# Kernel optimization log

Measured on AMD Instinct MI355X. Metric: run time of the kernel, lower is better.

The kernel has to match this reference:

```python
import jax, jax.numpy as jnp
import numpy as np

N_POINTS = 2_000_000
OUTPUT_DIM = 8
L_RES = 128
H_RES = 1024


def _to_idx(c, size):
    # c in [-1, 1], align_corners=True mapping to pixel coords
    p = (c + 1.0) * 0.5 * (size - 1)
    i0 = jnp.floor(p)
    w = p - i0  # interpolation weight toward i1
    i0 = jnp.clip(i0.astype(jnp.int32), 0, size - 1)
    i1 = jnp.clip(i0 + 1, 0, size - 1)
    return i0, i1, w


def trilinear_sample(grid, coords):
    # grid: [C, D, H, W]; coords: [N, 3] with (x->W, y->H, z->D); returns [C, N]
    C, D, H, W = grid.shape
    x0, x1, wx = _to_idx(coords[:, 0], W)
    y0, y1, wy = _to_idx(coords[:, 1], H)
    z0, z1, wz = _to_idx(coords[:, 2], D)
    g = lambda zi, yi, xi: grid[:, zi, yi, xi]  # gather -> [C, N]
    out = (g(z0, y0, x0) * ((1 - wz) * (1 - wy) * (1 - wx))
           + g(z0, y0, x1) * ((1 - wz) * (1 - wy) * wx)
           + g(z0, y1, x0) * ((1 - wz) * wy * (1 - wx))
           + g(z0, y1, x1) * ((1 - wz) * wy * wx)
           + g(z1, y0, x0) * (wz * (1 - wy) * (1 - wx))
           + g(z1, y0, x1) * (wz * (1 - wy) * wx)
           + g(z1, y1, x0) * (wz * wy * (1 - wx))
           + g(z1, y1, x1) * (wz * wy * wx))
    return out


def bilinear_sample(plane, coords):
    # plane: [C, H, W]; coords: [N, 2] with (x->W, y->H); returns [C, N]
    C, H, W = plane.shape
    x0, x1, wx = _to_idx(coords[:, 0], W)
    y0, y1, wy = _to_idx(coords[:, 1], H)
    g = lambda yi, xi: plane[:, yi, xi]  # [C, N]
    out = (g(y0, x0) * ((1 - wy) * (1 - wx))
           + g(y0, x1) * ((1 - wy) * wx)
           + g(y1, x0) * (wy * (1 - wx))
           + g(y1, x1) * (wy * wx))
    return out


def setup_inputs() -> dict:
    key = jax.random.key(0)
    k1, k2, k3 = jax.random.split(key, 3)
    xyz = jax.random.uniform(k1, (N_POINTS, 3), dtype=jnp.float32)  # in [0,1) subset of [-1,1]
    L_grid = jax.random.normal(k2, (1, OUTPUT_DIM, L_RES, L_RES, L_RES), dtype=jnp.float32) * 0.1
    H_planes = jax.random.normal(k3, (3, OUTPUT_DIM, H_RES, H_RES), dtype=jnp.float32) * 0.1
    return {"xyz": xyz, "bound": 1, "L_grid": L_grid, "H_planes": H_planes}


def reference(xyz, bound, L_grid, H_planes):
    xyz_norm = xyz / bound  # [N, 3]
    L_out = trilinear_sample(L_grid[0], xyz_norm)  # [C, N]
    H_out = (bilinear_sample(H_planes[0], xyz_norm[:, jnp.array([0, 1])])
             + bilinear_sample(H_planes[1], xyz_norm[:, jnp.array([1, 2])])
             + bilinear_sample(H_planes[2], xyz_norm[:, jnp.array([2, 0])]))
    return (L_out + H_out).T  # [N, C]
```

## Files before the change

### kernel.cpp

```cpp
#include <hip/hip_runtime.h>

#define LRES 128
#define HRES 1024
#define NB 256
#define BTS 1024
#define NBUCK 512
#define RCAP 8192
#define TELEM 2048

static const int LVOX = LRES * LRES * LRES;
static const int PPIX = HRES * HRES;
static const int TV = LVOX + 3 * PPIX;

typedef float f32x4 __attribute__((ext_vector_type(4)));
typedef unsigned u32x4 __attribute__((ext_vector_type(4)));


__device__ __forceinline__ void to_idx(float c, int size, int& i0, int& i1, float& w) {
    float p = (c + 1.0f) * 0.5f * (float)(size - 1);
    float f = floorf(p);
    w = p - f;
    int i = (int)f;
    i0 = min(max(i, 0), size - 1);
    i1 = min(i0 + 1, size - 1);
}

__device__ __forceinline__ unsigned f2bf(float f) {
    unsigned u = __float_as_uint(f);
    return (u + 0x7FFFu + ((u >> 16) & 1u)) >> 16;
}
__device__ __forceinline__ float bflo(unsigned u) { return __uint_as_float(u << 16); }
__device__ __forceinline__ float bfhi(unsigned u) { return __uint_as_float(u & 0xFFFF0000u); }

__device__ __forceinline__ void fma8u(f32x4& a0, f32x4& a1, uint4 q, float w) {
    a0.x = fmaf(bflo(q.x), w, a0.x);
    a0.y = fmaf(bfhi(q.x), w, a0.y);
    a0.z = fmaf(bflo(q.y), w, a0.z);
    a0.w = fmaf(bfhi(q.y), w, a0.w);
    a1.x = fmaf(bflo(q.z), w, a1.x);
    a1.y = fmaf(bfhi(q.z), w, a1.y);
    a1.z = fmaf(bflo(q.w), w, a1.z);
    a1.w = fmaf(bfhi(q.w), w, a1.w);
}

__device__ __forceinline__ unsigned spread3(unsigned x) {
    x &= 0x3FFu;
    x = (x | (x << 16)) & 0x030000FFu;
    x = (x | (x << 8)) & 0x0300F00Fu;
    x = (x | (x << 4)) & 0x030C30C3u;
    x = (x | (x << 2)) & 0x09249249u;
    return x;
}
__device__ __forceinline__ unsigned morton21(float x, float y, float z) {
    int px = min(max((int)(x * 128.f), 0), 127);
    int py = min(max((int)(y * 128.f), 0), 127);
    int pz = min(max((int)(z * 128.f), 0), 127);
    return spread3(px) | (spread3(py) << 1) | (spread3(pz) << 2);
}

__device__ __forceinline__ void gl_lds16(const float* src, float* lds_dst) {
    __builtin_amdgcn_global_load_lds(
        (const __attribute__((address_space(1))) void*)src,
        (__attribute__((address_space(3))) void*)lds_dst, 16, 0, 0);
}

__global__ __launch_bounds__(BTS) void hist_k(const float* __restrict__ xyz,
                                              const int* __restrict__ boundp,
                                              unsigned* __restrict__ hmat, int N) {
    __shared__ unsigned h[NBUCK];
    int b = blockIdx.x;
    for (int i = threadIdx.x; i < NBUCK; i += BTS) h[i] = 0u;
    __syncthreads();
    float invb = 1.0f / (float)boundp[0];
    int NG = (N + 3) >> 2;
    for (int g = b * BTS + threadIdx.x; g < NG; g += NB * BTS) {
        int n0 = g << 2;
        if (n0 + 4 <= N) {
            f32x4 qa = *(const f32x4*)(xyz + (size_t)n0 * 3);
            f32x4 qb = *(const f32x4*)(xyz + (size_t)n0 * 3 + 4);
            f32x4 qc = *(const f32x4*)(xyz + (size_t)n0 * 3 + 8);
            atomicAdd(&h[morton21(qa.x * invb, qa.y * invb, qa.z * invb) >> 12], 1u);
            atomicAdd(&h[morton21(qa.w * invb, qb.x * invb, qb.y * invb) >> 12], 1u);
            atomicAdd(&h[morton21(qb.z * invb, qb.w * invb, qc.x * invb) >> 12], 1u);
            atomicAdd(&h[morton21(qc.y * invb, qc.z * invb, qc.w * invb) >> 12], 1u);
        } else {
            for (int n = n0; n < N; ++n) {
                float x = xyz[(size_t)3 * n + 0] * invb;
                float y = xyz[(size_t)3 * n + 1] * invb;
                float z = xyz[(size_t)3 * n + 2] * invb;
                atomicAdd(&h[morton21(x, y, z) >> 12], 1u);
            }
        }
    }
    __syncthreads();
    for (int i = threadIdx.x; i < NBUCK; i += BTS)
        hmat[(size_t)i * NB + b] = h[i];
}

__global__ __launch_bounds__(1024) void offsets_k(unsigned* __restrict__ hmat,
                                                  unsigned* __restrict__ bb) {
    __shared__ unsigned tot[NBUCK];
    __shared__ unsigned cbase[NBUCK];
    int t = threadIdx.x;
    unsigned run = 0;
    if (t < NBUCK) {
        u32x4* row = (u32x4*)(hmat + (size_t)t * NB);
        for (int ch = 0; ch < NB / 32; ++ch) {
            u32x4 q[8];
#pragma unroll
            for (int k = 0; k < 8; ++k) q[k] = row[ch * 8 + k];
#pragma unroll
            for (int k = 0; k < 8; ++k) {
                unsigned v0 = q[k].x, v1 = q[k].y, v2 = q[k].z, v3 = q[k].w;
                q[k].x = run; run += v0;
                q[k].y = run; run += v1;
                q[k].z = run; run += v2;
                q[k].w = run; run += v3;
                row[ch * 8 + k] = q[k];
            }
        }
        tot[t] = run;
    }
    __syncthreads();
    for (int o = 1; o < NBUCK; o <<= 1) {
        unsigned v = 0;
        if (t < NBUCK && t >= o) v = tot[t - o];
        __syncthreads();
        if (t < NBUCK) tot[t] += v;
        __syncthreads();
    }
    if (t < NBUCK) {
        unsigned excl = tot[t] - run;
        cbase[t] = excl;
        bb[t] = excl;
        if (t == NBUCK - 1) bb[NBUCK] = tot[t];
    }
    __syncthreads();
    u32x4* hm4 = (u32x4*)hmat;
    for (int idx = t; idx < NB * NBUCK / 4; idx += 1024) {
        u32x4 q = hm4[idx];
        unsigned cb = cbase[idx >> 6];
        q.x += cb; q.y += cb; q.z += cb; q.w += cb;
        hm4[idx] = q;
    }
}

__global__ __launch_bounds__(BTS) void scat_tr_k(const float* __restrict__ xyz,
                                                 const int* __restrict__ boundp,
                                                 const float* __restrict__ Lg,
                                                 const float* __restrict__ Hp,
                                                 const unsigned* __restrict__ hmat,
                                                 float4* __restrict__ s1,
                                                 u32x4* __restrict__ gclb,
                                                 u32x4* __restrict__ pclb, int N) {
    __shared__ float stage[8 * TELEM];
    int b = blockIdx.x;
    if (b < NB) {
        unsigned* cnt = (unsigned*)stage;
        for (int i = threadIdx.x; i < NBUCK; i += BTS)
            cnt[i] = hmat[(size_t)i * NB + b];
        __syncthreads();
        float invb = 1.0f / (float)boundp[0];
        int NG = (N + 3) >> 2;
        for (int g = b * BTS + threadIdx.x; g < NG; g += NB * BTS) {
            int n0 = g << 2;
            if (n0 + 4 <= N) {
                f32x4 qa = *(const f32x4*)(xyz + (size_t)n0 * 3);
                f32x4 qb = *(const f32x4*)(xyz + (size_t)n0 * 3 + 4);
                f32x4 qc = *(const f32x4*)(xyz + (size_t)n0 * 3 + 8);
                {
                    float x = qa.x * invb, y = qa.y * invb, z = qa.z * invb;
                    unsigned d = atomicAdd(&cnt[morton21(x, y, z) >> 12], 1u);
                    s1[d] = make_float4(x, y, z, __int_as_float(n0 + 0));
                }
                {
                    float x = qa.w * invb, y = qb.x * invb, z = qb.y * invb;
                    unsigned d = atomicAdd(&cnt[morton21(x, y, z) >> 12], 1u);
                    s1[d] = make_float4(x, y, z, __int_as_float(n0 + 1));
                }
                {
                    float x = qb.z * invb, y = qb.w * invb, z = qc.x * invb;
                    unsigned d = atomicAdd(&cnt[morton21(x, y, z) >> 12], 1u);
                    s1[d] = make_float4(x, y, z, __int_as_float(n0 + 2));
                }
                {
                    float x = qc.y * invb, y = qc.z * invb, z = qc.w * invb;
                    unsigned d = atomicAdd(&cnt[morton21(x, y, z) >> 12], 1u);
                    s1[d] = make_float4(x, y, z, __int_as_float(n0 + 3));
                }
            } else {
                for (int n = n0; n < N; ++n) {
                    float x = xyz[(size_t)3 * n + 0] * invb;
                    float y = xyz[(size_t)3 * n + 1] * invb;
                    float z = xyz[(size_t)3 * n + 2] * invb;
                    unsigned d = atomicAdd(&cnt[morton21(x, y, z) >> 12], 1u);
                    s1[d] = make_float4(x, y, z, __int_as_float(n));
                }
            }
        }
    } else {
        int tb = b - NB;
        size_t vbase = (size_t)tb * TELEM;
        const float* srcbase;
        size_t cstride;
        u32x4* dst;
        if (vbase < (size_t)LVOX) {
            srcbase = Lg + vbase;
            cstride = LVOX;
            dst = gclb + vbase;
        } else {
            size_t u = vbase - LVOX;
            int p = (int)(u >> 20);
            size_t r = u & (size_t)(PPIX - 1);
            srcbase = Hp + (size_t)p * 8 * PPIX + r;
            cstride = PPIX;
            dst = pclb + (size_t)p * PPIX + r;
        }
        int wave = threadIdx.x >> 6;
        int lane = threadIdx.x & 63;
        for (int k = wave; k < 64; k += BTS / 64) {
            int c = k >> 3, s = k & 7;
            gl_lds16(srcbase + (size_t)c * cstride + s * 256 + lane * 4,
                     &stage[k * 256]);
        }
        __syncthreads();
        int t = threadIdx.x;
#pragma unroll
        for (int e = 0; e < TELEM / BTS; ++e) {
            int v = e * BTS + t;
            unsigned hc[8];
#pragma unroll
            for (int c = 0; c < 8; ++c) hc[c] = f2bf(stage[c * TELEM + v]);
            u32x4 o;
            o.x = hc[0] | (hc[1] << 16);
            o.y = hc[2] | (hc[3] << 16);
            o.z = hc[4] | (hc[5] << 16);
            o.w = hc[6] | (hc[7] << 16);
            dst[v] = o;
        }
    }
}

__global__ __launch_bounds__(1024) void refine_k(const float4* __restrict__ s1,
                                                 const unsigned* __restrict__ bb,
                                                 float4* __restrict__ s2) {
    __shared__ unsigned hist[4096];
    __shared__ unsigned part[1024];
    int b = blockIdx.x;
    unsigned start = bb[b];
    unsigned cnt = bb[b + 1] - start;
    int t = threadIdx.x;
    if (cnt > RCAP) {
        for (unsigned j = t; j < cnt; j += 1024) s2[start + j] = s1[start + j];
        return;
    }
    for (int i = t; i < 4096; i += 1024) hist[i] = 0u;
    __syncthreads();
    float4 rec[RCAP / 1024];
    unsigned key[RCAP / 1024], tick[RCAP / 1024];
#pragma unroll
    for (int k = 0; k < RCAP / 1024; ++k) {
        unsigned j = t + k * 1024u;
        if (j < cnt) {
            rec[k] = s1[start + j];
            key[k] = morton21(rec[k].x, rec[k].y, rec[k].z) & 4095u;
            tick[k] = atomicAdd(&hist[key[k]], 1u);
        }
    }
    __syncthreads();
    unsigned h4[4];
    unsigned s = 0;
#pragma unroll
    for (int k = 0; k < 4; ++k) {
        h4[k] = hist[t * 4 + k];
        s += h4[k];
    }
    part[t] = s;
    __syncthreads();
    for (int o = 1; o < 1024; o <<= 1) {
        unsigned v = (t >= o) ? part[t - o] : 0u;
        __syncthreads();
        part[t] += v;
        __syncthreads();
    }
    unsigned base = part[t] - s;
#pragma unroll
    for (int k = 0; k < 4; ++k) {
        hist[t * 4 + k] = base;
        base += h4[k];
    }
    __syncthreads();
#pragma unroll
    for (int k = 0; k < RCAP / 1024; ++k) {
        unsigned j = t + k * 1024u;
        if (j < cnt) s2[start + hist[key[k]] + tick[k]] = rec[k];
    }
}

__global__ __launch_bounds__(256) void sample_srt(const float4* __restrict__ sorted,
                                                  const uint4* __restrict__ gclb,
                                                  const uint4* __restrict__ pclb,
                                                  float* __restrict__ out, int N) {
    int i = blockIdx.x * blockDim.x + threadIdx.x;
    if (i >= N) return;
    float4 rec = sorted[i];
    float x = rec.x, y = rec.y, z = rec.z;
    int idx = __float_as_int(rec.w);

    int x0, x1, y0, y1, z0, z1;
    float wx, wy, wz;
    to_idx(x, LRES, x0, x1, wx);
    to_idx(y, LRES, y0, y1, wy);
    to_idx(z, LRES, z0, z1, wz);
    const uint4* b00 = gclb + ((size_t)z0 * LRES + y0) * LRES;
    const uint4* b01 = gclb + ((size_t)z0 * LRES + y1) * LRES;
    const uint4* b10 = gclb + ((size_t)z1 * LRES + y0) * LRES;
    const uint4* b11 = gclb + ((size_t)z1 * LRES + y1) * LRES;
    uint4 g0 = b00[x0], g1 = b00[x1], g2 = b01[x0], g3 = b01[x1];
    uint4 g4 = b10[x0], g5 = b10[x1], g6 = b11[x0], g7 = b11[x1];

    const float cw[3] = {x, y, z};
    const float ch[3] = {y, z, x};
    float pww[3], pwh[3];
    uint4 r[12];
#pragma unroll
    for (int p = 0; p < 3; ++p) {
        int w0, w1, h0, h1;
        to_idx(cw[p], HRES, w0, w1, pww[p]);
        to_idx(ch[p], HRES, h0, h1, pwh[p]);
        const uint4* base = pclb + (size_t)p * PPIX;
        const uint4* r0 = base + (size_t)h0 * HRES;
        const uint4* r1 = base + (size_t)h1 * HRES;
        r[4 * p + 0] = r0[w0];
        r[4 * p + 1] = r0[w1];
        r[4 * p + 2] = r1[w0];
        r[4 * p + 3] = r1[w1];
    }

    f32x4 a0 = (f32x4)0.f;
    f32x4 a1 = (f32x4)0.f;
    {
        float ux = 1.f - wx, uy = 1.f - wy, uz = 1.f - wz;
        fma8u(a0, a1, g0, uz * uy * ux);
        fma8u(a0, a1, g1, uz * uy * wx);
        fma8u(a0, a1, g2, uz * wy * ux);
        fma8u(a0, a1, g3, uz * wy * wx);
        fma8u(a0, a1, g4, wz * uy * ux);
        fma8u(a0, a1, g5, wz * uy * wx);
        fma8u(a0, a1, g6, wz * wy * ux);
        fma8u(a0, a1, g7, wz * wy * wx);
    }
#pragma unroll
    for (int p = 0; p < 3; ++p) {
        float ww = pww[p], wh = pwh[p];
        float uw = 1.f - ww, uh = 1.f - wh;
        fma8u(a0, a1, r[4 * p + 0], uh * uw);
        fma8u(a0, a1, r[4 * p + 1], uh * ww);
        fma8u(a0, a1, r[4 * p + 2], wh * uw);
        fma8u(a0, a1, r[4 * p + 3], wh * ww);
    }

    f32x4* o = (f32x4*)(out + (size_t)idx * 8);
    o[0] = a0;
    o[1] = a1;
}

__global__ __launch_bounds__(256) void sample_cf(
    const float* __restrict__ xyz, const int* __restrict__ boundp,
    const float* __restrict__ Lg, const float* __restrict__ Hp,
    float* __restrict__ out, int N) {
    int n = blockIdx.x * blockDim.x + threadIdx.x;
    if (n >= N) return;
    float invb = 1.0f / (float)boundp[0];
    float x = xyz[(size_t)3 * n + 0] * invb;
    float y = xyz[(size_t)3 * n + 1] * invb;
    float z = xyz[(size_t)3 * n + 2] * invb;
    float acc[8];
#pragma unroll
    for (int c = 0; c < 8; ++c) acc[c] = 0.f;
    {
        int x0, x1, y0, y1, z0, z1;
        float wx, wy, wz;
        to_idx(x, LRES, x0, x1, wx);
        to_idx(y, LRES, y0, y1, wy);
        to_idx(z, LRES, z0, z1, wz);
        float ux = 1.f - wx, uy = 1.f - wy, uz = 1.f - wz;
        size_t i8[8];
        i8[0] = ((size_t)z0 * LRES + y0) * LRES + x0;
        i8[1] = ((size_t)z0 * LRES + y0) * LRES + x1;
        i8[2] = ((size_t)z0 * LRES + y1) * LRES + x0;
        i8[3] = ((size_t)z0 * LRES + y1) * LRES + x1;
        i8[4] = ((size_t)z1 * LRES + y0) * LRES + x0;
        i8[5] = ((size_t)z1 * LRES + y0) * LRES + x1;
        i8[6] = ((size_t)z1 * LRES + y1) * LRES + x0;
        i8[7] = ((size_t)z1 * LRES + y1) * LRES + x1;
        float w8[8] = {uz * uy * ux, uz * uy * wx, uz * wy * ux, uz * wy * wx,
                       wz * uy * ux, wz * uy * wx, wz * wy * ux, wz * wy * wx};
#pragma unroll
        for (int c = 0; c < 8; ++c) {
            const float* g = Lg + (size_t)c * LVOX;
            float s = 0.f;
#pragma unroll
            for (int k = 0; k < 8; ++k) s = fmaf(g[i8[k]], w8[k], s);
            acc[c] += s;
        }
    }
    {
        const float cw[3] = {x, y, z};
        const float ch[3] = {y, z, x};
        for (int p = 0; p < 3; ++p) {
            int w0, w1, h0, h1;
            float ww, wh;
            to_idx(cw[p], HRES, w0, w1, ww);
            to_idx(ch[p], HRES, h0, h1, wh);
            float uw = 1.f - ww, uh = 1.f - wh;
            size_t i4[4] = {(size_t)h0 * HRES + w0, (size_t)h0 * HRES + w1,
                            (size_t)h1 * HRES + w0, (size_t)h1 * HRES + w1};
            float w4[4] = {uh * uw, uh * ww, wh * uw, wh * ww};
            const float* pb = Hp + (size_t)p * 8 * PPIX;
#pragma unroll
            for (int c = 0; c < 8; ++c) {
                const float* g = pb + (size_t)c * PPIX;
                float s = 0.f;
#pragma unroll
                for (int k = 0; k < 4; ++k) s = fmaf(g[i4[k]], w4[k], s);
                acc[c] += s;
            }
        }
    }
#pragma unroll
    for (int c = 0; c < 8; ++c) out[(size_t)n * 8 + c] = acc[c];
}

extern "C" void kernel_launch(void* const* d_in, const int* in_sizes, int n_in,
                              void* d_out, int out_size, void* d_ws, size_t ws_size,
                              hipStream_t stream) {
    const float* xyz = (const float*)d_in[0];
    const int* bound = (const int*)d_in[1];
    const float* Lg = (const float*)d_in[2];
    const float* Hp = (const float*)d_in[3];
    float* out = (float*)d_out;
    int N = in_sizes[0] / 3;

    size_t off = 0;
    size_t gclb_b = (size_t)LVOX * 16;
    size_t pclb_b = (size_t)3 * PPIX * 16;
    size_t s1_b = (size_t)N * 16;
    size_t s2_b = (size_t)N * 16;
    size_t hmat_b = (size_t)NB * NBUCK * 4;
    size_t bb_b = (size_t)(NBUCK + 1) * 4;
    size_t need = gclb_b + pclb_b + s1_b + s2_b + hmat_b + bb_b;

    if (ws_size >= need) {
        char* w = (char*)d_ws;
        u32x4* gclb = (u32x4*)(w + off);       off += gclb_b;
        u32x4* pclb = (u32x4*)(w + off);       off += pclb_b;
        float4* s1 = (float4*)(w + off);       off += s1_b;
        float4* s2 = (float4*)(w + off);       off += s2_b;
        unsigned* hmat = (unsigned*)(w + off); off += hmat_b;
        unsigned* bb = (unsigned*)(w + off);

        hist_k<<<NB, BTS, 0, stream>>>(xyz, bound, hmat, N);
        offsets_k<<<1, 1024, 0, stream>>>(hmat, bb);
        int st_blocks = NB + TV / TELEM;
        scat_tr_k<<<st_blocks, BTS, 0, stream>>>(xyz, bound, Lg, Hp, hmat, s1,
                                                 gclb, pclb, N);
        refine_k<<<NBUCK, 1024, 0, stream>>>(s1, bb, s2);
        sample_srt<<<(N + 255) / 256, 256, 0, stream>>>(s2, (const uint4*)gclb,
                                                        (const uint4*)pclb, out, N);
    } else {
        sample_cf<<<(N + 255) / 256, 256, 0, stream>>>(xyz, bound, Lg, Hp, out, N);
    }
}
```

Before: 429.8 us.

## Split grid transpose across histogram and scatter kernels; parallelize bucket offset scan

Moves part of the grid/plane bf16 transpose tiles into the histogram kernel so they overlap with histogramming, leaving the rest for the scatter kernel. It also replaces the single-block offsets kernel with a per-bucket wave-shuffle prefix kernel plus a small 512-thread scan, adding the global base inside the scatter kernel. This is meant to remove the serial single-block offsets bottleneck and balance work between the two prep kernels, at the cost of one extra launch.

```diff
diff --git a/kernel.cpp b/kernel.cpp
--- a/kernel.cpp
+++ b/kernel.cpp
@@ -7,6 +7,8 @@
 #define NBUCK 512
 #define RCAP 8192
 #define TELEM 2048
+#define TILES_A 1408
+#define TILES_B 1152
 
 static const int LVOX = LRES * LRES * LRES;
 static const int PPIX = HRES * HRES;
@@ -64,101 +66,149 @@
         (__attribute__((address_space(3))) void*)lds_dst, 16, 0, 0);
 }
 
-__global__ __launch_bounds__(BTS) void hist_k(const float* __restrict__ xyz,
-                                              const int* __restrict__ boundp,
-                                              unsigned* __restrict__ hmat, int N) {
-    __shared__ unsigned h[NBUCK];
+
+__device__ __forceinline__ void transpose_tile(int tile, const float* __restrict__ Lg,
+                                               const float* __restrict__ Hp,
+                                               u32x4* __restrict__ gclb,
+                                               u32x4* __restrict__ pclb,
+                                               float* stage) {
+    size_t vbase = (size_t)tile * TELEM;
+    const float* srcbase;
+    size_t cstride;
+    u32x4* dst;
+    if (vbase < (size_t)LVOX) {
+        srcbase = Lg + vbase;
+        cstride = LVOX;
+        dst = gclb + vbase;
+    } else {
+        size_t u = vbase - LVOX;
+        int p = (int)(u >> 20);
+        size_t r = u & (size_t)(PPIX - 1);
+        srcbase = Hp + (size_t)p * 8 * PPIX + r;
+        cstride = PPIX;
+        dst = pclb + (size_t)p * PPIX + r;
+    }
+    int wave = threadIdx.x >> 6;
+    int lane = threadIdx.x & 63;
+    for (int k = wave; k < 64; k += BTS / 64) {
+        int c = k >> 3, s = k & 7;
+        gl_lds16(srcbase + (size_t)c * cstride + s * 256 + lane * 4,
+                 &stage[k * 256]);
+    }
+    __syncthreads();
+    int t = threadIdx.x;
+#pragma unroll
+    for (int e = 0; e < TELEM / BTS; ++e) {
+        int v = e * BTS + t;
+        unsigned hc[8];
+#pragma unroll
+        for (int c = 0; c < 8; ++c) hc[c] = f2bf(stage[c * TELEM + v]);
+        u32x4 o;
+        o.x = hc[0] | (hc[1] << 16);
+        o.y = hc[2] | (hc[3] << 16);
+        o.z = hc[4] | (hc[5] << 16);
+        o.w = hc[6] | (hc[7] << 16);
+        dst[v] = o;
+    }
+}
+
+__global__ __launch_bounds__(BTS) void prep1_k(const float* __restrict__ xyz,
+                                               const int* __restrict__ boundp,
+                                               const float* __restrict__ Lg,
+                                               const float* __restrict__ Hp,
+                                               unsigned* __restrict__ hmat,
+                                               u32x4* __restrict__ gclb,
+                                               u32x4* __restrict__ pclb, int N) {
+    __shared__ float stage[8 * TELEM];
     int b = blockIdx.x;
-    for (int i = threadIdx.x; i < NBUCK; i += BTS) h[i] = 0u;
-    __syncthreads();
-    float invb = 1.0f / (float)boundp[0];
-    int NG = (N + 3) >> 2;
-    for (int g = b * BTS + threadIdx.x; g < NG; g += NB * BTS) {
-        int n0 = g << 2;
-        if (n0 + 4 <= N) {
-            f32x4 qa = *(const f32x4*)(xyz + (size_t)n0 * 3);
-            f32x4 qb = *(const f32x4*)(xyz + (size_t)n0 * 3 + 4);
-            f32x4 qc = *(const f32x4*)(xyz + (size_t)n0 * 3 + 8);
-            atomicAdd(&h[morton21(qa.x * invb, qa.y * invb, qa.z * invb) >> 12], 1u);
-            atomicAdd(&h[morton21(qa.w * invb, qb.x * invb, qb.y * invb) >> 12], 1u);
-            atomicAdd(&h[morton21(qb.z * invb, qb.w * invb, qc.x * invb) >> 12], 1u);
-            atomicAdd(&h[morton21(qc.y * invb, qc.z * invb, qc.w * invb) >> 12], 1u);
-        } else {
-            for (int n = n0; n < N; ++n) {
-                float x = xyz[(size_t)3 * n + 0] * invb;
-                float y = xyz[(size_t)3 * n + 1] * invb;
-                float z = xyz[(size_t)3 * n + 2] * invb;
-                atomicAdd(&h[morton21(x, y, z) >> 12], 1u);
+    if (b < NB) {
+        unsigned* h = (unsigned*)stage;
+        for (int i = threadIdx.x; i < NBUCK; i += BTS) h[i] = 0u;
+        __syncthreads();
+        float invb = 1.0f / (float)boundp[0];
+        int NG = (N + 3) >> 2;
+        for (int g = b * BTS + threadIdx.x; g < NG; g += NB * BTS) {
+            int n0 = g << 2;
+            if (n0 + 4 <= N) {
+                f32x4 qa = *(const f32x4*)(xyz + (size_t)n0 * 3);
+                f32x4 qb = *(const f32x4*)(xyz + (size_t)n0 * 3 + 4);
+                f32x4 qc = *(const f32x4*)(xyz + (size_t)n0 * 3 + 8);
+                atomicAdd(&h[morton21(qa.x * invb, qa.y * invb, qa.z * invb) >> 12], 1u);
+                atomicAdd(&h[morton21(qa.w * invb, qb.x * invb, qb.y * invb) >> 12], 1u);
+                atomicAdd(&h[morton21(qb.z * invb, qb.w * invb, qc.x * invb) >> 12], 1u);
+                atomicAdd(&h[morton21(qc.y * invb, qc.z * invb, qc.w * invb) >> 12], 1u);
+            } else {
+                for (int n = n0; n < N; ++n) {
+                    float x = xyz[(size_t)3 * n + 0] * invb;
+                    float y = xyz[(size_t)3 * n + 1] * invb;
+                    float z = xyz[(size_t)3 * n + 2] * invb;
+                    atomicAdd(&h[morton21(x, y, z) >> 12], 1u);
+                }
             }
         }
-    }
-    __syncthreads();
-    for (int i = threadIdx.x; i < NBUCK; i += BTS)
-        hmat[(size_t)i * NB + b] = h[i];
-}
-
-__global__ __launch_bounds__(1024) void offsets_k(unsigned* __restrict__ hmat,
-                                                  unsigned* __restrict__ bb) {
+        __syncthreads();
+        for (int i = threadIdx.x; i < NBUCK; i += BTS)
+            hmat[(size_t)i * NB + b] = h[i];
+    } else {
+        transpose_tile(b - NB, Lg, Hp, gclb, pclb, stage);
+    }
+}
+
+__global__ __launch_bounds__(64) void colpfx_k(unsigned* __restrict__ hmat,
+                                               unsigned* __restrict__ tt) {
+    int bucket = blockIdx.x;
+    int lane = threadIdx.x;
+    u32x4* row = (u32x4*)(hmat + (size_t)bucket * NB);
+    u32x4 q = row[lane];
+    unsigned sum = q.x + q.y + q.z + q.w;
+    unsigned inc = sum;
+#pragma unroll
+    for (int o = 1; o < 64; o <<= 1) {
+        unsigned v = __shfl_up(inc, o, 64);
+        if (lane >= o) inc += v;
+    }
+    unsigned base = inc - sum;
+    u32x4 o4;
+    o4.x = base; base += q.x;
+    o4.y = base; base += q.y;
+    o4.z = base; base += q.z;
+    o4.w = base;
+    row[lane] = o4;
+    if (lane == 63) tt[bucket] = inc;
+}
+
+__global__ __launch_bounds__(NBUCK) void scan_k(const unsigned* __restrict__ tt,
+                                                unsigned* __restrict__ bb) {
     __shared__ unsigned tot[NBUCK];
-    __shared__ unsigned cbase[NBUCK];
     int t = threadIdx.x;
-    unsigned run = 0;
-    if (t < NBUCK) {
-        u32x4* row = (u32x4*)(hmat + (size_t)t * NB);
-        for (int ch = 0; ch < NB / 32; ++ch) {
-            u32x4 q[8];
-#pragma unroll
-            for (int k = 0; k < 8; ++k) q[k] = row[ch * 8 + k];
-#pragma unroll
-            for (int k = 0; k < 8; ++k) {
-                unsigned v0 = q[k].x, v1 = q[k].y, v2 = q[k].z, v3 = q[k].w;
-                q[k].x = run; run += v0;
-                q[k].y = run; run += v1;
-                q[k].z = run; run += v2;
-                q[k].w = run; run += v3;
-                row[ch * 8 + k] = q[k];
-            }
-        }
-        tot[t] = run;
-    }
+    unsigned own = tt[t];
+    tot[t] = own;
     __syncthreads();
     for (int o = 1; o < NBUCK; o <<= 1) {
-        unsigned v = 0;
-        if (t < NBUCK && t >= o) v = tot[t - o];
-        __syncthreads();
-        if (t < NBUCK) tot[t] += v;
-        __syncthreads();
-    }
-    if (t < NBUCK) {
-        unsigned excl = tot[t] - run;
-        cbase[t] = excl;
-        bb[t] = excl;
-        if (t == NBUCK - 1) bb[NBUCK] = tot[t];
-    }
-    __syncthreads();
-    u32x4* hm4 = (u32x4*)hmat;
-    for (int idx = t; idx < NB * NBUCK / 4; idx += 1024) {
-        u32x4 q = hm4[idx];
-        unsigned cb = cbase[idx >> 6];
-        q.x += cb; q.y += cb; q.z += cb; q.w += cb;
-        hm4[idx] = q;
-    }
-}
-
-__global__ __launch_bounds__(BTS) void scat_tr_k(const float* __restrict__ xyz,
-                                                 const int* __restrict__ boundp,
-                                                 const float* __restrict__ Lg,
-                                                 const float* __restrict__ Hp,
-                                                 const unsigned* __restrict__ hmat,
-                                                 float4* __restrict__ s1,
-                                                 u32x4* __restrict__ gclb,
-                                                 u32x4* __restrict__ pclb, int N) {
+        unsigned v = (t >= o) ? tot[t - o] : 0u;
+        __syncthreads();
+        tot[t] += v;
+        __syncthreads();
+    }
+    bb[t] = tot[t] - own;
+    if (t == NBUCK - 1) bb[NBUCK] = tot[t];
+}
+
+__global__ __launch_bounds__(BTS) void prep2_k(const float* __restrict__ xyz,
+                                               const int* __restrict__ boundp,
+                                               const float* __restrict__ Lg,
+                                               const float* __restrict__ Hp,
+                                               const unsigned* __restrict__ hmat,
+                                               const unsigned* __restrict__ bb,
+                                               float4* __restrict__ s1,
+                                               u32x4* __restrict__ gclb,
+                                               u32x4* __restrict__ pclb, int N) {
     __shared__ float stage[8 * TELEM];
     int b = blockIdx.x;
     if (b < NB) {
         unsigned* cnt = (unsigned*)stage;
         for (int i = threadIdx.x; i < NBUCK; i += BTS)
-            cnt[i] = hmat[(size_t)i * NB + b];
+            cnt[i] = hmat[(size_t)i * NB + b] + bb[i];
         __syncthreads();
         float invb = 1.0f / (float)boundp[0];
         int NG = (N + 3) >> 2;
@@ -199,45 +249,7 @@
             }
         }
     } else {
-        int tb = b - NB;
-        size_t vbase = (size_t)tb * TELEM;
-        const float* srcbase;
-        size_t cstride;
-        u32x4* dst;
-        if (vbase < (size_t)LVOX) {
-            srcbase = Lg + vbase;
-            cstride = LVOX;
-            dst = gclb + vbase;
-        } else {
-            size_t u = vbase - LVOX;
-            int p = (int)(u >> 20);
-            size_t r = u & (size_t)(PPIX - 1);
-            srcbase = Hp + (size_t)p * 8 * PPIX + r;
-            cstride = PPIX;
-            dst = pclb + (size_t)p * PPIX + r;
-        }
-        int wave = threadIdx.x >> 6;
-        int lane = threadIdx.x & 63;
-        for (int k = wave; k < 64; k += BTS / 64) {
-            int c = k >> 3, s = k & 7;
-            gl_lds16(srcbase + (size_t)c * cstride + s * 256 + lane * 4,
-                     &stage[k * 256]);
-        }
-        __syncthreads();
-        int t = threadIdx.x;
-#pragma unroll
-        for (int e = 0; e < TELEM / BTS; ++e) {
-            int v = e * BTS + t;
-            unsigned hc[8];
-#pragma unroll
-            for (int c = 0; c < 8; ++c) hc[c] = f2bf(stage[c * TELEM + v]);
-            u32x4 o;
-            o.x = hc[0] | (hc[1] << 16);
-            o.y = hc[2] | (hc[3] << 16);
-            o.z = hc[4] | (hc[5] << 16);
-            o.w = hc[6] | (hc[7] << 16);
-            dst[v] = o;
-        }
+        transpose_tile(TILES_A + (b - NB), Lg, Hp, gclb, pclb, stage);
     }
 }
 
@@ -449,7 +461,8 @@
     size_t s2_b = (size_t)N * 16;
     size_t hmat_b = (size_t)NB * NBUCK * 4;
     size_t bb_b = (size_t)(NBUCK + 1) * 4;
-    size_t need = gclb_b + pclb_b + s1_b + s2_b + hmat_b + bb_b;
+    size_t tt_b = (size_t)NBUCK * 4;
+    size_t need = gclb_b + pclb_b + s1_b + s2_b + hmat_b + bb_b + tt_b;
 
     if (ws_size >= need) {
         char* w = (char*)d_ws;
@@ -458,13 +471,15 @@
         float4* s1 = (float4*)(w + off);       off += s1_b;
         float4* s2 = (float4*)(w + off);       off += s2_b;
         unsigned* hmat = (unsigned*)(w + off); off += hmat_b;
-        unsigned* bb = (unsigned*)(w + off);
-
-        hist_k<<<NB, BTS, 0, stream>>>(xyz, bound, hmat, N);
-        offsets_k<<<1, 1024, 0, stream>>>(hmat, bb);
-        int st_blocks = NB + TV / TELEM;
-        scat_tr_k<<<st_blocks, BTS, 0, stream>>>(xyz, bound, Lg, Hp, hmat, s1,
-                                                 gclb, pclb, N);
+        unsigned* bb = (unsigned*)(w + off);   off += bb_b;
+        unsigned* tt = (unsigned*)(w + off);
+
+        prep1_k<<<NB + TILES_A, BTS, 0, stream>>>(xyz, bound, Lg, Hp, hmat,
+                                                  gclb, pclb, N);
+        colpfx_k<<<NBUCK, 64, 0, stream>>>(hmat, tt);
+        scan_k<<<1, NBUCK, 0, stream>>>(tt, bb);
+        prep2_k<<<NB + TILES_B, BTS, 0, stream>>>(xyz, bound, Lg, Hp, hmat, bb,
+                                                  s1, gclb, pclb, N);
         refine_k<<<NBUCK, 1024, 0, stream>>>(s1, bb, s2);
         sample_srt<<<(N + 255) / 256, 256, 0, stream>>>(s2, (const uint4*)gclb,
                                                         (const uint4*)pclb, out, N);
```

After: 379.5 us. 1.13x faster.
